# Optimization experiments

Hardware: AMD Instinct MI355X
Metric: run time of the kernel (lower is better)

The kernel has to match this reference:

```python
import jax, jax.numpy as jnp
import numpy as np

N = 20000      # nodes
E = 640000     # edges (avg degree 32)
IN = 32        # input_dim
HID = 256      # hidden_dim
H = 8          # num_heads
Dh = HID // H  # head_dim = 32
TD = 32        # time_dim
L = 3          # num_layers
OUT = 2


def setup_inputs() -> dict:
    key = jax.random.key(0)
    ks = jax.random.split(key, 20)
    def w(k, sh):
        return (jax.random.normal(k, sh, jnp.float32) * 0.05)
    return {
        "x": jax.random.normal(ks[0], (N, IN), jnp.float32),
        "timestamps": jax.random.uniform(ks[1], (N,), jnp.float32),
        "edge_index": jax.random.randint(ks[2], (2, E), 0, N, jnp.int32),
        "batch": jnp.zeros((N,), jnp.int32),
        "time_freq": jax.random.normal(ks[3], (TD // 2,), jnp.float32),
        "inW": w(ks[4], (IN, HID)), "inb": jnp.zeros((HID,), jnp.float32),
        "qW": w(ks[5], (L, HID + TD, HID)), "qb": jnp.zeros((L, HID), jnp.float32),
        "kW": w(ks[6], (L, HID + TD, HID)), "kb": jnp.zeros((L, HID), jnp.float32),
        "vW": w(ks[7], (L, HID, HID)), "vb": jnp.zeros((L, HID), jnp.float32),
        "oW": w(ks[8], (L, HID, HID)), "ob": jnp.zeros((L, HID), jnp.float32),
        "c1W": w(ks[9], (HID, HID // 2)), "c1b": jnp.zeros((HID // 2,), jnp.float32),
        "c2W": w(ks[10], (HID // 2, OUT)), "c2b": jnp.zeros((OUT,), jnp.float32),
    }


def reference(x, timestamps, time_freq, inW, inb, qW, qb, kW, kb, vW, vb,
              oW, ob, c1W, c1b, c2W, c2b, edge_index, batch):
    n = x.shape[0]
    src, dst = edge_index[0], edge_index[1]

    # Functional time encoding (node-level timestamps branch)
    t = (timestamps - timestamps.min()) / (timestamps.max() - timestamps.min() + 1e-8)
    wt = t[:, None] * time_freq[None, :]                      # [N, TD/2]
    tf = jnp.concatenate([jnp.cos(wt), jnp.sin(wt)], axis=-1)  # [N, TD]

    h = x @ inW + inb                                          # [N, HID]
    scale = 1.0 / np.sqrt(Dh).astype(np.float32)

    for l in range(L):
        xt = jnp.concatenate([h, tf], axis=-1)                 # [N, HID+TD]
        Q = (xt @ qW[l] + qb[l]).reshape(n, H, Dh)
        K = (xt @ kW[l] + kb[l]).reshape(n, H, Dh)
        V = (h @ vW[l] + vb[l]).reshape(n, H, Dh)

        # per-edge attention scores [E, H]
        scores = jnp.einsum('ehd,ehd->eh', Q[dst], K[src]) * scale

        # segment softmax over incoming edges of each dst node
        m = jax.ops.segment_max(scores, dst, num_segments=n)   # [N, H]
        e = jnp.exp(scores - m[dst])
        s = jax.ops.segment_sum(e, dst, num_segments=n)        # [N, H]
        att = e / s[dst]                                       # [E, H]

        msgs = att[..., None] * V[src]                         # [E, H, Dh]
        out = jax.ops.segment_sum(msgs, dst, num_segments=n)   # [N, H, Dh]
        out = out.reshape(n, HID) @ oW[l] + ob[l]
        h = jax.nn.elu(out)

    # global mean pool (single graph: batch all zeros)
    cnt = jax.ops.segment_sum(jnp.ones((n, 1), h.dtype), batch, num_segments=1)
    g = jax.ops.segment_sum(h, batch, num_segments=1) / jnp.maximum(cnt, 1.0)

    logits = jax.nn.relu(g @ c1W + c1b) @ c2W + c2b            # [1, OUT]
    return logits
```

## Files before the change

kernel.cpp:

```cpp
#include <hip/hip_runtime.h>
#include <math.h>

#define HID 256
#define TD 32
#define NL 3
#define C1DIM 128
#define OUTDIM 2
#define QKVW 768

using half8  = __attribute__((ext_vector_type(8))) _Float16;
using half4v = __attribute__((ext_vector_type(4))) _Float16;
using half2v = __attribute__((ext_vector_type(2))) _Float16;
using f32x4  = __attribute__((ext_vector_type(4))) float;

typedef __attribute__((address_space(1))) void gbl_void_t;
typedef __attribute__((address_space(3))) void lds_void_t;

__device__ __forceinline__ void load16_to_lds(const void* g, void* l) {
  __builtin_amdgcn_global_load_lds((const gbl_void_t*)g, (lds_void_t*)l, 16, 0, 0);
}

__device__ __forceinline__ float dot8h(half8 a, half8 b, float acc) {
#if __has_builtin(__builtin_amdgcn_fdot2)
  union { half8 v; half2v h2[4]; } ua, ub;
  ua.v = a; ub.v = b;
#pragma unroll
  for (int j = 0; j < 4; ++j) acc = __builtin_amdgcn_fdot2(ua.h2[j], ub.h2[j], acc, false);
  return acc;
#else
#pragma unroll
  for (int j = 0; j < 8; ++j) acc += (float)a[j] * (float)b[j];
  return acc;
#endif
}

__global__ __launch_bounds__(1024) void k_tsmm(const float* __restrict__ ts,
                                               float* __restrict__ mmf,
                                               int* __restrict__ deg, int n) {
  int t = threadIdx.x;
  float lmin = INFINITY, lmax = -INFINITY;
  for (int i = t; i < n; i += 1024) {
    float v = ts[i];
    lmin = fminf(lmin, v);
    lmax = fmaxf(lmax, v);
    deg[i] = 0;
  }
#pragma unroll
  for (int off = 32; off >= 1; off >>= 1) {
    lmin = fminf(lmin, __shfl_xor(lmin, off));
    lmax = fmaxf(lmax, __shfl_xor(lmax, off));
  }
  __shared__ float wmin[16], wmax[16];
  int lane = t & 63, w = t >> 6;
  if (lane == 0) { wmin[w] = lmin; wmax[w] = lmax; }
  __syncthreads();
  if (t == 0) {
    float a = INFINITY, b = -INFINITY;
    for (int i = 0; i < 16; ++i) { a = fminf(a, wmin[i]); b = fmaxf(b, wmax[i]); }
    mmf[0] = a; mmf[1] = b;
  }
}

__global__ void k_enc(const float* __restrict__ ts, const float* __restrict__ freq,
                      const float* __restrict__ mmf, const float* __restrict__ x,
                      _Float16* __restrict__ tfh, _Float16* __restrict__ xh, int n) {
  int idx = blockIdx.x * blockDim.x + threadIdx.x;
  int nt = n * TD;
  if (idx < nt) {
    int node = idx >> 5, j = idx & 31;
    float t = (ts[node] - mmf[0]) / (mmf[1] - mmf[0] + 1e-8f);
    float w = t * freq[j & 15];
    tfh[idx] = (_Float16)((j < 16) ? cosf(w) : sinf(w));
  } else if (idx < nt + n * 32) {
    int i2 = idx - nt;
    xh[i2] = (_Float16)x[i2];
  }
}

__global__ void k_prep(const float* __restrict__ qW,
                       const float* __restrict__ kW, const float* __restrict__ vW,
                       const float* __restrict__ oW, const float* __restrict__ qb,
                       const float* __restrict__ kb, const float* __restrict__ vb,
                       _Float16* __restrict__ qkvWt,
                       float* __restrict__ qkvb, _Float16* __restrict__ oWt) {
  int idx = blockIdx.x * blockDim.x + threadIdx.x;
  const int KQ = HID + TD;
  const int S1 = NL * QKVW * KQ;
  const int S2 = NL * QKVW;
  const int S3 = NL * HID * HID;
  if (idx < S1) {
    int l = idx / (QKVW * KQ);
    int rem = idx - l * (QKVW * KQ);
    int nrow = rem / KQ;
    int k = rem - nrow * KQ;
    float v;
    if (nrow < 256)      v = qW[(size_t)l * KQ * HID + (size_t)k * HID + nrow];
    else if (nrow < 512) v = kW[(size_t)l * KQ * HID + (size_t)k * HID + (nrow - 256)];
    else                 v = (k < HID) ? vW[(size_t)l * HID * HID + (size_t)k * HID + (nrow - 512)] : 0.f;
    qkvWt[idx] = (_Float16)v;
  } else if ((idx -= S1) < S2) {
    int l = idx / QKVW;
    int j = idx - l * QKVW;
    float v;
    if (j < 256)      v = qb[l * HID + j];
    else if (j < 512) v = kb[l * HID + (j - 256)];
    else              v = vb[l * HID + (j - 512)];
    qkvb[idx] = v;
  } else if ((idx -= S2) < S3) {
    int l = idx / (HID * HID);
    int rem = idx - l * (HID * HID);
    int nrow = rem / HID;
    int k = rem - nrow * HID;
    oWt[idx] = (_Float16)oW[(size_t)l * HID * HID + (size_t)k * HID + nrow];
  }
}

__global__ __launch_bounds__(256) void k_fold(const float* __restrict__ inW,
                                              const float* __restrict__ inb,
                                              const float* __restrict__ qW,
                                              const float* __restrict__ kW,
                                              const float* __restrict__ vW,
                                              const float* __restrict__ qb,
                                              const float* __restrict__ kb,
                                              const float* __restrict__ vb,
                                              _Float16* __restrict__ WcT,
                                              float* __restrict__ bc) {
  int idx = blockIdx.x * 256 + threadIdx.x;
  if (idx >= 65 * QKVW) return;
  int j = idx / QKVW;
  int nrow = idx - j * QKVW;
  const int KQ = HID + TD;
  auto W0 = [&](int c, int nr) -> float {
    if (nr < 256)      return qW[(size_t)c * HID + nr];
    else if (nr < 512) return kW[(size_t)c * HID + (nr - 256)];
    else               return vW[(size_t)c * HID + (nr - 512)];
  };
  if (j < 32) {
    float acc = 0.f;
    for (int c = 0; c < 256; ++c) acc += inW[j * HID + c] * W0(c, nrow);
    WcT[(size_t)nrow * 64 + j] = (_Float16)acc;
  } else if (j < 64) {
    int r = 256 + (j - 32);
    float v = 0.f;
    if (nrow < 256)      v = qW[(size_t)r * HID + nrow];
    else if (nrow < 512) v = kW[(size_t)r * HID + (nrow - 256)];
    WcT[(size_t)nrow * 64 + j] = (_Float16)v;
  } else {
    float acc;
    if (nrow < 256)      acc = qb[nrow];
    else if (nrow < 512) acc = kb[nrow - 256];
    else                 acc = vb[nrow - 512];
    for (int c = 0; c < 256; ++c) acc += inb[c] * W0(c, nrow);
    bc[nrow] = acc;
  }
}

__global__ void k_count(const int* __restrict__ dst, int* deg, int e) {
  int i = blockIdx.x * blockDim.x + threadIdx.x;
  if (i < e) atomicAdd(&deg[dst[i]], 1);
}

__global__ __launch_bounds__(256) void k_scan_part(const int* __restrict__ deg,
                                                   int* __restrict__ bsum, int n) {
  int t = threadIdx.x;
  int idx = blockIdx.x * 256 + t;
  int v = (idx < n) ? deg[idx] : 0;
  int lane = t & 63, w = t >> 6;
  int x = v;
#pragma unroll
  for (int off = 1; off < 64; off <<= 1) {
    int y = __shfl_up(x, off);
    if (lane >= off) x += y;
  }
  __shared__ int ws[4];
  if (lane == 63) ws[w] = x;
  __syncthreads();
  if (t == 0) bsum[blockIdx.x] = ws[0] + ws[1] + ws[2] + ws[3];
}

__global__ __launch_bounds__(64) void k_scan_mid(const int* __restrict__ bsum,
                                                 int* __restrict__ boff, int nb) {
  int lane = threadIdx.x;
  int carry = 0;
  for (int base = 0; base < nb; base += 64) {
    int i = base + lane;
    int v = (i < nb) ? bsum[i] : 0;
    int x = v;
#pragma unroll
    for (int off = 1; off < 64; off <<= 1) {
      int y = __shfl_up(x, off);
      if (lane >= off) x += y;
    }
    if (i < nb) boff[i] = carry + x - v;
    carry += __shfl(x, 63);
  }
}

__global__ __launch_bounds__(256) void k_scan_apply(const int* __restrict__ deg,
                                                    const int* __restrict__ boff,
                                                    int* __restrict__ row_ptr,
                                                    int* __restrict__ cursor, int n, int e) {
  int t = threadIdx.x;
  int idx = blockIdx.x * 256 + t;
  int v = (idx < n) ? deg[idx] : 0;
  int lane = t & 63, w = t >> 6;
  int x = v;
#pragma unroll
  for (int off = 1; off < 64; off <<= 1) {
    int y = __shfl_up(x, off);
    if (lane >= off) x += y;
  }
  __shared__ int ws[4];
  if (lane == 63) ws[w] = x;
  __syncthreads();
  int wpre = 0;
  for (int i = 0; i < w; ++i) wpre += ws[i];
  if (idx < n) {
    row_ptr[idx] = boff[blockIdx.x] + wpre + x - v;
    cursor[idx] = 0;
  }
  if (idx == 0) row_ptr[n] = e;
}

__global__ void k_scatter(const int* __restrict__ src, const int* __restrict__ dst,
                          const int* __restrict__ row_ptr, int* cursor,
                          int* __restrict__ colbuf, int e) {
  int i = blockIdx.x * blockDim.x + threadIdx.x;
  if (i >= e) return;
  int d = dst[i];
  int p = atomicAdd(&cursor[d], 1);
  colbuf[row_ptr[d] + p] = src[i];
}

__global__ __launch_bounds__(256) void k_gemm_f16(
    const _Float16* __restrict__ A1, int K1,
    const _Float16* __restrict__ A2, int K2,
    const _Float16* __restrict__ Bt,
    const float* __restrict__ bias,
    _Float16* __restrict__ C,
    _Float16* __restrict__ Qb,
    _Float16* __restrict__ KV,
    int M, int Ncols, int Ktot, int mode) {
  __shared__ half8 smem8[2 * 768];
  char* smem = (char*)smem8;
  const int tid = threadIdx.x;
  const int lane = tid & 63, wave = tid >> 6;
  const int wm = wave >> 1, wn = wave & 1;
  const int row0 = blockIdx.y * 128;
  const int col0 = blockIdx.x * 64;

  auto stage = [&](int buf, int k0) {
    char* sA = smem + buf * 12288;
    char* sB = sA + 8192;
#pragma unroll
    for (int i = 0; i < 2; ++i) {
      int kg = i * 2 + (wave >> 1);
      int row = (wave & 1) * 64 + lane;
      int grow = row0 + row; if (grow > M - 1) grow = M - 1;
      int k = k0 + kg * 8;
      const _Float16* src = (k < K1) ? (A1 + (size_t)grow * K1 + k)
                                     : (A2 + (size_t)grow * K2 + (k - K1));
      load16_to_lds(src, sA + (i * 256 + wave * 64) * 16);
    }
    {
      const _Float16* src = Bt + (size_t)(col0 + lane) * Ktot + k0 + wave * 8;
      load16_to_lds(src, sB + wave * 64 * 16);
    }
  };

  f32x4 acc[4][2];
#pragma unroll
  for (int mf = 0; mf < 4; ++mf)
#pragma unroll
    for (int nf = 0; nf < 2; ++nf) acc[mf][nf] = f32x4{0.f, 0.f, 0.f, 0.f};

  const int nsteps = Ktot >> 5;
  int cur = 0;
  stage(0, 0);
  __syncthreads();
  for (int st = 0; st < nsteps; ++st) {
    if (st + 1 < nsteps) stage(cur ^ 1, (st + 1) * 32);
    char* sA = smem + cur * 12288;
    char* sB = sA + 8192;
    half8 af[4], bf[2];
#pragma unroll
    for (int mf = 0; mf < 4; ++mf) {
      int slot = (lane >> 4) * 128 + wm * 64 + mf * 16 + (lane & 15);
      af[mf] = *(const half8*)(sA + slot * 16);
    }
#pragma unroll
    for (int nf = 0; nf < 2; ++nf) {
      int slot = (lane >> 4) * 64 + wn * 32 + nf * 16 + (lane & 15);
      bf[nf] = *(const half8*)(sB + slot * 16);
    }
#pragma unroll
    for (int mf = 0; mf < 4; ++mf)
#pragma unroll
      for (int nf = 0; nf < 2; ++nf)
        acc[mf][nf] = __builtin_amdgcn_mfma_f32_16x16x32_f16(af[mf], bf[nf], acc[mf][nf], 0, 0, 0);
    __syncthreads();
    cur ^= 1;
  }

  const int rbase = row0 + wm * 64 + (lane >> 4) * 4;
  const int cbase = col0 + wn * 32 + (lane & 15);
#pragma unroll
  for (int nf = 0; nf < 2; ++nf) {
    int col = cbase + nf * 16;
    float bv = bias[col];
    if (mode != 2) {
#pragma unroll
      for (int mf = 0; mf < 4; ++mf) {
#pragma unroll
        for (int r = 0; r < 4; ++r) {
          int row = rbase + mf * 16 + r;
          if (row < M) {
            float v = acc[mf][nf][r] + bv;
            if (mode == 1) v = (v > 0.f) ? v : expm1f(v);
            C[(size_t)row * Ncols + col] = (_Float16)v;
          }
        }
      }
    } else {
      bool isQ = col < 256;
      int cc = col - 256;
      int isV = cc >> 8;
      int c2 = cc & 255;
      int hh = c2 >> 5, dim = c2 & 31;
      size_t kvoff = ((size_t)hh * M) * 64 + isV * 32 + dim;
#pragma unroll
      for (int mf = 0; mf < 4; ++mf) {
#pragma unroll
        for (int r = 0; r < 4; ++r) {
          int row = rbase + mf * 16 + r;
          if (row < M) {
            float v = acc[mf][nf][r] + bv;
            if (isQ) Qb[(size_t)row * HID + col] = (_Float16)v;
            else     KV[kvoff + (size_t)row * 64] = (_Float16)v;
          }
        }
      }
    }
  }
}

__global__ __launch_bounds__(256) void k_attn(const _Float16* __restrict__ Qb,
                                              const _Float16* __restrict__ KV,
                                              const int* __restrict__ row_ptr,
                                              const int* __restrict__ colbuf,
                                              _Float16* __restrict__ out, int n) {
  int h = blockIdx.x & 7;
  int node = (blockIdx.x >> 3) * 64 + (threadIdx.x >> 2);
  if (node >= n) return;
  int j = threadIdx.x & 3;
  const float scale = 0.17677669529663687f;
  const _Float16* KVh = KV + ((size_t)h * n) * 64;

  half8 qh = *(const half8*)(Qb + (size_t)node * HID + h * 32 + j * 8);
  half8 qs;
#pragma unroll
  for (int q = 0; q < 8; ++q) qs[q] = (_Float16)((float)qh[q] * scale);

  int beg = row_ptr[node], end = row_ptr[node + 1];
  float m = -INFINITY, s = 0.f;
  float a[8] = {0.f, 0.f, 0.f, 0.f, 0.f, 0.f, 0.f, 0.f};

  for (int i = beg; i < end; i += 4) {
    half8 kk[4], vv[4];
#pragma unroll
    for (int t = 0; t < 4; ++t) {
      int ii = i + t; if (ii > end - 1) ii = end - 1;
      int sn = colbuf[ii];
      const _Float16* b = KVh + ((size_t)sn) * 64 + j * 8;
      kk[t] = *(const half8*)(b);
      vv[t] = *(const half8*)(b + 32);
    }
    float p[4];
#pragma unroll
    for (int t = 0; t < 4; ++t) p[t] = dot8h(qs, kk[t], 0.f);
#pragma unroll
    for (int t = 0; t < 4; ++t) {
      p[t] += __shfl_xor(p[t], 1);
      p[t] += __shfl_xor(p[t], 2);
      if (i + t >= end) p[t] = -INFINITY;
    }
#pragma unroll
    for (int t = 0; t < 4; ++t) {
      float sc_ = p[t];
      if (sc_ <= m) {
        float e2 = __expf(sc_ - m);
        s += e2;
#pragma unroll
        for (int q = 0; q < 8; ++q) a[q] = fmaf(e2, (float)vv[t][q], a[q]);
      } else {
        float f = __expf(m - sc_);
        s = s * f + 1.f;
#pragma unroll
        for (int q = 0; q < 8; ++q) a[q] = fmaf(a[q], f, (float)vv[t][q]);
        m = sc_;
      }
    }
  }

  float inv = (s > 0.f) ? (1.f / s) : 0.f;
  half8 o;
#pragma unroll
  for (int q = 0; q < 8; ++q) o[q] = (_Float16)(a[q] * inv);
  *(half8*)(out + (size_t)node * HID + h * 32 + j * 8) = o;
}

__global__ __launch_bounds__(256) void k_pool_partial(const _Float16* __restrict__ h,
                                                      float* __restrict__ partial, int n) {
  int b = blockIdx.x, t = threadIdx.x;
  float s = 0.f;
  for (int r = b; r < n; r += 256) s += (float)h[(size_t)r * HID + t];
  partial[b * HID + t] = s;
}

__global__ __launch_bounds__(256) void k_final(const float* __restrict__ partial,
                                               const float* __restrict__ c1W,
                                               const float* __restrict__ c1b,
                                               const float* __restrict__ c2W,
                                               const float* __restrict__ c2b,
                                               float* __restrict__ out, int n) {
  __shared__ float gl[HID];
  __shared__ float r1[C1DIM];
  int t = threadIdx.x;
  float s = 0.f;
  for (int b = 0; b < 256; b++) s += partial[b * HID + t];
  gl[t] = s / (float)n;
  __syncthreads();
  if (t < C1DIM) {
    float a = c1b[t];
    for (int k = 0; k < HID; k++) a += gl[k] * c1W[k * C1DIM + t];
    r1[t] = fmaxf(a, 0.f);
  }
  __syncthreads();
  if (t < OUTDIM) {
    float a = c2b[t];
    for (int k = 0; k < C1DIM; k++) a += r1[k] * c2W[k * OUTDIM + t];
    out[t] = a;
  }
}

extern "C" void kernel_launch(void* const* d_in, const int* in_sizes, int n_in,
                              void* d_out, int out_size, void* d_ws, size_t ws_size,
                              hipStream_t stream) {
  const float* x    = (const float*)d_in[0];
  const float* ts   = (const float*)d_in[1];
  const int*   ei   = (const int*)d_in[2];
  const float* freq = (const float*)d_in[4];
  const float* inW  = (const float*)d_in[5];
  const float* inb  = (const float*)d_in[6];
  const float* qW   = (const float*)d_in[7];
  const float* qb   = (const float*)d_in[8];
  const float* kW   = (const float*)d_in[9];
  const float* kb   = (const float*)d_in[10];
  const float* vW   = (const float*)d_in[11];
  const float* vb   = (const float*)d_in[12];
  const float* oW   = (const float*)d_in[13];
  const float* ob   = (const float*)d_in[14];
  const float* c1W  = (const float*)d_in[15];
  const float* c1b  = (const float*)d_in[16];
  const float* c2W  = (const float*)d_in[17];
  const float* c2b  = (const float*)d_in[18];

  int n = in_sizes[1];
  int e = in_sizes[2] / 2;
  const int* src = ei;
  const int* dst = ei + e;
  int nb = (n + 255) / 256;

  char* w = (char*)d_ws;
  size_t off = 0;
  auto alloc = [&](size_t bytes) -> char* {
    char* p = w + off;
    off = (off + bytes + 255) & ~(size_t)255;
    return p;
  };
  _Float16* tfh     = (_Float16*)alloc((size_t)n * TD * 2);
  _Float16* xh      = (_Float16*)alloc((size_t)n * 32 * 2);
  _Float16* h       = (_Float16*)alloc((size_t)n * HID * 2);
  _Float16* Qbuf    = (_Float16*)alloc((size_t)n * HID * 2);
  _Float16* KV      = (_Float16*)alloc((size_t)n * 512 * 2);
  _Float16* ao      = (_Float16*)alloc((size_t)n * HID * 2);
  _Float16* qkvWt   = (_Float16*)alloc((size_t)NL * QKVW * (HID + TD) * 2);
  float*    qkvb    = (float*)alloc((size_t)NL * QKVW * 4);
  _Float16* oWt     = (_Float16*)alloc((size_t)NL * HID * HID * 2);
  _Float16* WcT     = (_Float16*)alloc((size_t)QKVW * 64 * 2);
  float*    bc      = (float*)alloc((size_t)QKVW * 4);
  int*      deg     = (int*)alloc((size_t)n * 4);
  int*      cursor  = (int*)alloc((size_t)n * 4);
  int*      row_ptr = (int*)alloc((size_t)(n + 1) * 4);
  int*      colbuf  = (int*)alloc((size_t)e * 4);
  int*      bsum    = (int*)alloc((size_t)nb * 4);
  int*      boff    = (int*)alloc((size_t)nb * 4);
  float*    partial = (float*)alloc((size_t)256 * HID * 4);
  float*    mmf     = (float*)alloc(256);

  int b256 = 256;
  hipLaunchKernelGGL(k_tsmm, dim3(1), dim3(1024), 0, stream, ts, mmf, deg, n);
  hipLaunchKernelGGL(k_enc, dim3((n * 64 + 255) / 256), dim3(b256), 0, stream,
                     ts, freq, mmf, x, tfh, xh, n);
  {
    int total = NL * QKVW * (HID + TD) + NL * QKVW + NL * HID * HID;
    hipLaunchKernelGGL(k_prep, dim3((total + 255) / 256), dim3(b256), 0, stream,
                       qW, kW, vW, oW, qb, kb, vb, qkvWt, qkvb, oWt);
  }
  hipLaunchKernelGGL(k_fold, dim3((65 * QKVW + 255) / 256), dim3(b256), 0, stream,
                     inW, inb, qW, kW, vW, qb, kb, vb, WcT, bc);
  hipLaunchKernelGGL(k_count, dim3((e + 255) / 256), dim3(b256), 0, stream, dst, deg, e);
  hipLaunchKernelGGL(k_scan_part, dim3(nb), dim3(b256), 0, stream, deg, bsum, n);
  hipLaunchKernelGGL(k_scan_mid, dim3(1), dim3(64), 0, stream, bsum, boff, nb);
  hipLaunchKernelGGL(k_scan_apply, dim3(nb), dim3(b256), 0, stream, deg, boff, row_ptr, cursor, n, e);
  hipLaunchKernelGGL(k_scatter, dim3((e + 255) / 256), dim3(b256), 0, stream, src, dst, row_ptr, cursor, colbuf, e);

  dim3 ggrid_h(HID / 64, (n + 127) / 128);
  dim3 ggrid_qkv(QKVW / 64, (n + 127) / 128);
  int nchunks = (n + 63) / 64;
  for (int l = 0; l < NL; ++l) {
    const float*    qkvbl  = qkvb + (size_t)l * QKVW;
    const _Float16* oWtl   = oWt + (size_t)l * HID * HID;
    if (l == 0) {
      hipLaunchKernelGGL(k_gemm_f16, ggrid_qkv, dim3(b256), 0, stream,
                         xh, 32, tfh, 32, WcT, bc, (_Float16*)nullptr, Qbuf, KV,
                         n, QKVW, 64, 2);
    } else {
      const _Float16* qkvWtl = qkvWt + (size_t)l * QKVW * (HID + TD);
      hipLaunchKernelGGL(k_gemm_f16, ggrid_qkv, dim3(b256), 0, stream,
                         h, HID, tfh, TD, qkvWtl, qkvbl, (_Float16*)nullptr, Qbuf, KV,
                         n, QKVW, HID + TD, 2);
    }
    hipLaunchKernelGGL(k_attn, dim3(nchunks * 8), dim3(b256), 0, stream,
                       Qbuf, KV, row_ptr, colbuf, ao, n);
    hipLaunchKernelGGL(k_gemm_f16, ggrid_h, dim3(b256), 0, stream,
                       ao, HID, ao, HID, oWtl, ob + l * HID, h, (_Float16*)nullptr, (_Float16*)nullptr,
                       n, HID, HID, 1);
  }

  hipLaunchKernelGGL(k_pool_partial, dim3(256), dim3(b256), 0, stream, h, partial, n);
  hipLaunchKernelGGL(k_final, dim3(1), dim3(b256), 0, stream, partial, c1W, c1b, c2W, c2b, (float*)d_out, n);
}
```

Baseline: 461.0 us.

## Use 128x32-tile QKV GEMM with XCD-aware block mapping and LDS-transposed weight prep

```diff
diff --git a/kernel.cpp b/kernel.cpp
--- a/kernel.cpp
+++ b/kernel.cpp
@@ -9,7 +9,6 @@
 #define QKVW 768
 
 using half8  = __attribute__((ext_vector_type(8))) _Float16;
-using half4v = __attribute__((ext_vector_type(4))) _Float16;
 using half2v = __attribute__((ext_vector_type(2))) _Float16;
 using f32x4  = __attribute__((ext_vector_type(4))) float;
 
@@ -77,41 +76,86 @@
   }
 }
 
-__global__ void k_prep(const float* __restrict__ qW,
-                       const float* __restrict__ kW, const float* __restrict__ vW,
-                       const float* __restrict__ oW, const float* __restrict__ qb,
-                       const float* __restrict__ kb, const float* __restrict__ vb,
-                       _Float16* __restrict__ qkvWt,
-                       float* __restrict__ qkvb, _Float16* __restrict__ oWt) {
-  int idx = blockIdx.x * blockDim.x + threadIdx.x;
+#define NB_QKV (NL * 9 * 12)
+#define NB_O   (NL * 8 * 4)
+#define NB_B   9
+
+__global__ __launch_bounds__(256) void k_prep2(
+    const float* __restrict__ qW, const float* __restrict__ kW,
+    const float* __restrict__ vW, const float* __restrict__ oW,
+    const float* __restrict__ qb, const float* __restrict__ kb,
+    const float* __restrict__ vb,
+    _Float16* __restrict__ qkvWt, float* __restrict__ qkvb,
+    _Float16* __restrict__ oWt) {
+  __shared__ _Float16 lds[32][65];
+  int bid = blockIdx.x;
+  int t = threadIdx.x;
   const int KQ = HID + TD;
-  const int S1 = NL * QKVW * KQ;
-  const int S2 = NL * QKVW;
-  const int S3 = NL * HID * HID;
-  if (idx < S1) {
-    int l = idx / (QKVW * KQ);
-    int rem = idx - l * (QKVW * KQ);
-    int nrow = rem / KQ;
-    int k = rem - nrow * KQ;
-    float v;
-    if (nrow < 256)      v = qW[(size_t)l * KQ * HID + (size_t)k * HID + nrow];
-    else if (nrow < 512) v = kW[(size_t)l * KQ * HID + (size_t)k * HID + (nrow - 256)];
-    else                 v = (k < HID) ? vW[(size_t)l * HID * HID + (size_t)k * HID + (nrow - 512)] : 0.f;
-    qkvWt[idx] = (_Float16)v;
-  } else if ((idx -= S1) < S2) {
-    int l = idx / QKVW;
-    int j = idx - l * QKVW;
-    float v;
-    if (j < 256)      v = qb[l * HID + j];
-    else if (j < 512) v = kb[l * HID + (j - 256)];
-    else              v = vb[l * HID + (j - 512)];
-    qkvb[idx] = v;
-  } else if ((idx -= S2) < S3) {
-    int l = idx / (HID * HID);
-    int rem = idx - l * (HID * HID);
-    int nrow = rem / HID;
-    int k = rem - nrow * HID;
-    oWt[idx] = (_Float16)oW[(size_t)l * HID * HID + (size_t)k * HID + nrow];
+
+  if (bid < NB_QKV) {
+    int l = bid / 108;
+    int rem = bid - l * 108;
+    int kt = rem / 12, ntile = rem - kt * 12;
+    int k0 = kt * 32, n0 = ntile * 64;
+#pragma unroll
+    for (int it = 0; it < 8; ++it) {
+      int i = it * 256 + t;
+      int kk = i >> 6, nn = i & 63;
+      int k = k0 + kk, nrow = n0 + nn;
+      float v;
+      if (nrow < 256)      v = qW[(size_t)l * KQ * HID + (size_t)k * HID + nrow];
+      else if (nrow < 512) v = kW[(size_t)l * KQ * HID + (size_t)k * HID + (nrow - 256)];
+      else                 v = (k < HID) ? vW[(size_t)l * HID * HID + (size_t)k * HID + (nrow - 512)] : 0.f;
+      lds[kk][nn] = (_Float16)v;
+    }
+    __syncthreads();
+    {
+      int nn = t >> 2, kq = (t & 3) * 8;
+      _Float16* dst = qkvWt + (size_t)l * QKVW * KQ + (size_t)(n0 + nn) * KQ + k0 + kq;
+      half8 v;
+#pragma unroll
+      for (int j = 0; j < 8; ++j) v[j] = lds[kq + j][nn];
+      *(half8*)dst = v;
+    }
+    return;
+  }
+  bid -= NB_QKV;
+
+  if (bid < NB_O) {
+    int l = bid / 32;
+    int rem = bid - l * 32;
+    int kt = rem / 4, ntile = rem - kt * 4;
+    int k0 = kt * 32, n0 = ntile * 64;
+#pragma unroll
+    for (int it = 0; it < 8; ++it) {
+      int i = it * 256 + t;
+      int kk = i >> 6, nn = i & 63;
+      lds[kk][nn] = (_Float16)oW[(size_t)l * HID * HID + (size_t)(k0 + kk) * HID + n0 + nn];
+    }
+    __syncthreads();
+    {
+      int nn = t >> 2, kq = (t & 3) * 8;
+      _Float16* dst = oWt + (size_t)l * HID * HID + (size_t)(n0 + nn) * HID + k0 + kq;
+      half8 v;
+#pragma unroll
+      for (int j = 0; j < 8; ++j) v[j] = lds[kq + j][nn];
+      *(half8*)dst = v;
+    }
+    return;
+  }
+  bid -= NB_O;
+
+  {
+    int idx = bid * 256 + t;
+    if (idx < NL * QKVW) {
+      int l = idx / QKVW;
+      int j = idx - l * QKVW;
+      float v;
+      if (j < 256)      v = qb[l * HID + j];
+      else if (j < 512) v = kb[l * HID + (j - 256)];
+      else              v = vb[l * HID + (j - 512)];
+      qkvb[idx] = v;
+    }
   }
 }
 
@@ -129,7 +173,6 @@
   if (idx >= 65 * QKVW) return;
   int j = idx / QKVW;
   int nrow = idx - j * QKVW;
-  const int KQ = HID + TD;
   auto W0 = [&](int c, int nr) -> float {
     if (nr < 256)      return qW[(size_t)c * HID + nr];
     else if (nr < 512) return kW[(size_t)c * HID + (nr - 256)];
@@ -238,8 +281,6 @@
     const _Float16* __restrict__ Bt,
     const float* __restrict__ bias,
     _Float16* __restrict__ C,
-    _Float16* __restrict__ Qb,
-    _Float16* __restrict__ KV,
     int M, int Ncols, int Ktot, int mode) {
   __shared__ half8 smem8[2 * 768];
   char* smem = (char*)smem8;
@@ -308,35 +349,115 @@
   for (int nf = 0; nf < 2; ++nf) {
     int col = cbase + nf * 16;
     float bv = bias[col];
-    if (mode != 2) {
-#pragma unroll
-      for (int mf = 0; mf < 4; ++mf) {
-#pragma unroll
-        for (int r = 0; r < 4; ++r) {
-          int row = rbase + mf * 16 + r;
-          if (row < M) {
-            float v = acc[mf][nf][r] + bv;
-            if (mode == 1) v = (v > 0.f) ? v : expm1f(v);
-            C[(size_t)row * Ncols + col] = (_Float16)v;
-          }
+#pragma unroll
+    for (int mf = 0; mf < 4; ++mf) {
+#pragma unroll
+      for (int r = 0; r < 4; ++r) {
+        int row = rbase + mf * 16 + r;
+        if (row < M) {
+          float v = acc[mf][nf][r] + bv;
+          if (mode == 1) v = (v > 0.f) ? v : expm1f(v);
+          C[(size_t)row * Ncols + col] = (_Float16)v;
         }
       }
-    } else {
-      bool isQ = col < 256;
-      int cc = col - 256;
-      int isV = cc >> 8;
-      int c2 = cc & 255;
-      int hh = c2 >> 5, dim = c2 & 31;
-      size_t kvoff = ((size_t)hh * M) * 64 + isV * 32 + dim;
-#pragma unroll
-      for (int mf = 0; mf < 4; ++mf) {
-#pragma unroll
-        for (int r = 0; r < 4; ++r) {
-          int row = rbase + mf * 16 + r;
-          if (row < M) {
-            float v = acc[mf][nf][r] + bv;
-            if (isQ) Qb[(size_t)row * HID + col] = (_Float16)v;
-            else     KV[kvoff + (size_t)row * 64] = (_Float16)v;
+    }
+  }
+}
+
+__global__ __launch_bounds__(256) void k_gemm_qkv32(
+    const _Float16* __restrict__ A1, int K1,
+    const _Float16* __restrict__ A2, int K2,
+    const _Float16* __restrict__ Bt,
+    const float* __restrict__ bias,
+    _Float16* __restrict__ Qb,
+    _Float16* __restrict__ KV,
+    int M, int Ktot, int R) {
+  __shared__ half8 smem8[2 * 640];
+  char* smem = (char*)smem8;
+  int b = blockIdx.x;
+  int xcd = b & 7;
+  int idx = b >> 3;
+  int rowt, colt;
+  if (idx < 2 * R) { rowt = idx >> 1; colt = 8 + xcd + 8 * (idx & 1); }
+  else             { rowt = idx - 2 * R; colt = xcd; }
+  const int row0 = rowt * 128;
+  const int col0 = colt * 32;
+  const int tid = threadIdx.x;
+  const int lane = tid & 63, wave = tid >> 6;
+
+  auto stage = [&](int buf, int k0) {
+    char* sA = smem + buf * 10240;
+    char* sB = sA + 8192;
+#pragma unroll
+    for (int i = 0; i < 2; ++i) {
+      int kg = i * 2 + (wave >> 1);
+      int row = (wave & 1) * 64 + lane;
+      int grow = row0 + row; if (grow > M - 1) grow = M - 1;
+      int k = k0 + kg * 8;
+      const _Float16* src = (k < K1) ? (A1 + (size_t)grow * K1 + k)
+                                     : (A2 + (size_t)grow * K2 + (k - K1));
+      load16_to_lds(src, sA + (i * 256 + wave * 64) * 16);
+    }
+    if (lane < 32) {
+      const _Float16* src = Bt + (size_t)(col0 + lane) * Ktot + k0 + wave * 8;
+      load16_to_lds(src, sB + (wave * 32 + lane) * 16);
+    }
+  };
+
+  f32x4 acc[2][2];
+#pragma unroll
+  for (int mf = 0; mf < 2; ++mf)
+#pragma unroll
+    for (int nf = 0; nf < 2; ++nf) acc[mf][nf] = f32x4{0.f, 0.f, 0.f, 0.f};
+
+  const int nsteps = Ktot >> 5;
+  int cur = 0;
+  stage(0, 0);
+  __syncthreads();
+  for (int st = 0; st < nsteps; ++st) {
+    if (st + 1 < nsteps) stage(cur ^ 1, (st + 1) * 32);
+    char* sA = smem + cur * 10240;
+    char* sB = sA + 8192;
+    half8 af[2], bf[2];
+#pragma unroll
+    for (int mf = 0; mf < 2; ++mf) {
+      int slot = (lane >> 4) * 128 + wave * 32 + mf * 16 + (lane & 15);
+      af[mf] = *(const half8*)(sA + slot * 16);
+    }
+#pragma unroll
+    for (int nf = 0; nf < 2; ++nf) {
+      int slot = (lane >> 4) * 32 + nf * 16 + (lane & 15);
+      bf[nf] = *(const half8*)(sB + slot * 16);
+    }
+#pragma unroll
+    for (int mf = 0; mf < 2; ++mf)
+#pragma unroll
+      for (int nf = 0; nf < 2; ++nf)
+        acc[mf][nf] = __builtin_amdgcn_mfma_f32_16x16x32_f16(af[mf], bf[nf], acc[mf][nf], 0, 0, 0);
+    __syncthreads();
+    cur ^= 1;
+  }
+
+  const int rbase = row0 + wave * 32 + (lane >> 4) * 4;
+  const int lcol = lane & 15;
+#pragma unroll
+  for (int nf = 0; nf < 2; ++nf) {
+    int cg = col0 + nf * 16 + lcol;
+    float bv = bias[cg];
+    int dim = nf * 16 + lcol + (col0 & 31);
+#pragma unroll
+    for (int mf = 0; mf < 2; ++mf) {
+#pragma unroll
+      for (int r = 0; r < 4; ++r) {
+        int row = rbase + mf * 16 + r;
+        if (row < M) {
+          float v = acc[mf][nf][r] + bv;
+          if (colt < 8) {
+            Qb[(size_t)row * HID + cg] = (_Float16)v;
+          } else {
+            int isV = colt >= 16;
+            int hh = colt - (isV ? 16 : 8);
+            KV[((size_t)hh * M + row) * 64 + isV * 32 + dim] = (_Float16)v;
           }
         }
       }
@@ -470,6 +591,7 @@
   const int* src = ei;
   const int* dst = ei + e;
   int nb = (n + 255) / 256;
+  int R = (n + 127) / 128;
 
   char* w = (char*)d_ws;
   size_t off = 0;
@@ -502,11 +624,8 @@
   hipLaunchKernelGGL(k_tsmm, dim3(1), dim3(1024), 0, stream, ts, mmf, deg, n);
   hipLaunchKernelGGL(k_enc, dim3((n * 64 + 255) / 256), dim3(b256), 0, stream,
                      ts, freq, mmf, x, tfh, xh, n);
-  {
-    int total = NL * QKVW * (HID + TD) + NL * QKVW + NL * HID * HID;
-    hipLaunchKernelGGL(k_prep, dim3((total + 255) / 256), dim3(b256), 0, stream,
-                       qW, kW, vW, oW, qb, kb, vb, qkvWt, qkvb, oWt);
-  }
+  hipLaunchKernelGGL(k_prep2, dim3(NB_QKV + NB_O + NB_B), dim3(b256), 0, stream,
+                     qW, kW, vW, oW, qb, kb, vb, qkvWt, qkvb, oWt);
   hipLaunchKernelGGL(k_fold, dim3((65 * QKVW + 255) / 256), dim3(b256), 0, stream,
                      inW, inb, qW, kW, vW, qb, kb, vb, WcT, bc);
   hipLaunchKernelGGL(k_count, dim3((e + 255) / 256), dim3(b256), 0, stream, dst, deg, e);
@@ -516,26 +635,22 @@
   hipLaunchKernelGGL(k_scatter, dim3((e + 255) / 256), dim3(b256), 0, stream, src, dst, row_ptr, cursor, colbuf, e);
 
   dim3 ggrid_h(HID / 64, (n + 127) / 128);
-  dim3 ggrid_qkv(QKVW / 64, (n + 127) / 128);
   int nchunks = (n + 63) / 64;
   for (int l = 0; l < NL; ++l) {
-    const float*    qkvbl  = qkvb + (size_t)l * QKVW;
-    const _Float16* oWtl   = oWt + (size_t)l * HID * HID;
+    const float*    qkvbl = qkvb + (size_t)l * QKVW;
+    const _Float16* oWtl  = oWt + (size_t)l * HID * HID;
     if (l == 0) {
-      hipLaunchKernelGGL(k_gemm_f16, ggrid_qkv, dim3(b256), 0, stream,
-                         xh, 32, tfh, 32, WcT, bc, (_Float16*)nullptr, Qbuf, KV,
-                         n, QKVW, 64, 2);
+      hipLaunchKernelGGL(k_gemm_qkv32, dim3(24 * R), dim3(b256), 0, stream,
+                         xh, 32, tfh, 32, WcT, bc, Qbuf, KV, n, 64, R);
     } else {
       const _Float16* qkvWtl = qkvWt + (size_t)l * QKVW * (HID + TD);
-      hipLaunchKernelGGL(k_gemm_f16, ggrid_qkv, dim3(b256), 0, stream,
-                         h, HID, tfh, TD, qkvWtl, qkvbl, (_Float16*)nullptr, Qbuf, KV,
-                         n, QKVW, HID + TD, 2);
+      hipLaunchKernelGGL(k_gemm_qkv32, dim3(24 * R), dim3(b256), 0, stream,
+                         h, HID, tfh, TD, qkvWtl, qkvbl, Qbuf, KV, n, HID + TD, R);
     }
     hipLaunchKernelGGL(k_attn, dim3(nchunks * 8), dim3(b256), 0, stream,
                        Qbuf, KV, row_ptr, colbuf, ao, n);
     hipLaunchKernelGGL(k_gemm_f16, ggrid_h, dim3(b256), 0, stream,
-                       ao, HID, ao, HID, oWtl, ob + l * HID, h, (_Float16*)nullptr, (_Float16*)nullptr,
-                       n, HID, HID, 1);
+                       ao, HID, ao, HID, oWtl, ob + l * HID, h, n, HID, HID, 1);
   }
 
   hipLaunchKernelGGL(k_pool_partial, dim3(256), dim3(b256), 0, stream, h, partial, n);
```

Measured after the change: 490.7 us. +6.5%, slower.
